# Kernel optimization log

Hardware: AMD Instinct MI355X
Metric: run time of the kernel (lower is better)

The kernel has to match this reference:

```python
import jax, jax.numpy as jnp
import numpy as np

R_MIN, R_MAX, MAX_PHASE = 0.9, 0.999, 6.283
BN_EPS = 1e-5


def _lru(x, nu_log, theta_log, B_re, B_im, C_re, C_im, D):
    # x: [B,T,E]; diagonal LRU with complex state of size H
    lam = jnp.exp(-jnp.exp(nu_log) + 1j * jnp.exp(theta_log))          # [H] complex
    gamma = jnp.sqrt(jnp.maximum(1.0 - jnp.abs(lam) ** 2, 1e-12))      # [H]
    Bc = B_re + 1j * B_im                                               # [H,E]
    Cc = C_re + 1j * C_im                                               # [E,H]
    Bu = jnp.einsum('bte,he->bth', x.astype(jnp.complex64), Bc) * gamma  # [B,T,H]

    def step(h, u):
        h = lam * h + u
        return h, h

    h0 = jnp.zeros((x.shape[0], lam.shape[0]), jnp.complex64)
    _, hs = jax.lax.scan(step, h0, jnp.swapaxes(Bu, 0, 1))              # [T,B,H]
    hs = jnp.swapaxes(hs, 0, 1)                                         # [B,T,H]
    return jnp.einsum('bth,eh->bte', hs, Cc).real + D * x               # [B,T,E]


def _batchnorm(x, scale, bias):
    # normalize over (batch, time), feature axis last
    mu = jnp.mean(x, axis=(0, 1))
    var = jnp.var(x, axis=(0, 1))
    return (x - mu) * jax.lax.rsqrt(var + BN_EPS) * scale + bias


def _glu(x):
    a, b = jnp.split(x, 2, axis=-1)
    return a * jax.nn.sigmoid(b)


def setup_inputs() -> dict:
    key = jax.random.key(0)
    ks = jax.random.split(key, 16)
    B, T, TS, E, H, L, O, NB = 32, 2048, 64, 256, 256, 1024, 10, 6
    u1 = jax.random.uniform(ks[0], (NB, H))
    u2 = jax.random.uniform(ks[1], (NB, H))
    nu_log = jnp.log(-0.5 * jnp.log(u1 * (R_MAX**2 - R_MIN**2) + R_MIN**2))
    theta_log = jnp.log(MAX_PHASE * u2)
    return {
        'x': jax.random.normal(ks[2], (B, T, TS), jnp.float32),
        'W_enc': jax.random.normal(ks[3], (TS, E), jnp.float32) / np.sqrt(TS),
        'b_enc': jnp.zeros((E,), jnp.float32),
        'nu_log': nu_log.astype(jnp.float32),
        'theta_log': theta_log.astype(jnp.float32),
        'B_re': jax.random.normal(ks[4], (NB, H, E), jnp.float32) / np.sqrt(2 * E),
        'B_im': jax.random.normal(ks[5], (NB, H, E), jnp.float32) / np.sqrt(2 * E),
        'C_re': jax.random.normal(ks[6], (NB, E, H), jnp.float32) / np.sqrt(H),
        'C_im': jax.random.normal(ks[7], (NB, E, H), jnp.float32) / np.sqrt(H),
        'D': jax.random.normal(ks[8], (NB, E), jnp.float32),
        'W1': jax.random.normal(ks[9], (NB, E, L), jnp.float32) / np.sqrt(E),
        'b1': jnp.zeros((NB, L), jnp.float32),
        'W2': jax.random.normal(ks[10], (NB, L // 2, E), jnp.float32) / np.sqrt(L // 2),
        'b2': jnp.zeros((NB, E), jnp.float32),
        'bn_scale': jnp.ones((NB, E), jnp.float32),
        'bn_bias': jnp.zeros((NB, E), jnp.float32),
        'W_out': jax.random.normal(ks[11], (E, O), jnp.float32) / np.sqrt(E),
        'b_out': jnp.zeros((O,), jnp.float32),
    }


def reference(x, W_enc, b_enc, nu_log, theta_log, B_re, B_im, C_re, C_im, D,
              W1, b1, W2, b2, bn_scale, bn_bias, W_out, b_out):
    x = x @ W_enc + b_enc                      # [B,T,E]
    y = x                                       # residual anchor (same for every block)
    for i in range(6):
        h = _batchnorm(x, bn_scale[i], bn_bias[i])
        h = _lru(h, nu_log[i], theta_log[i], B_re[i], B_im[i], C_re[i], C_im[i], D[i])
        h = _glu(h @ W1[i] + b1[i])             # dropout is identity (p=0 / eval)
        h = h @ W2[i] + b2[i]
        x = h + y
    pooled = jnp.mean(x, axis=1)                # pool=True head: mean over time
    return pooled @ W_out + b_out               # [B, out_dim]
```

## Files before the change

### kernel.cpp

```cpp
#include <hip/hip_runtime.h>
#include <hip/hip_bf16.h>
#include <math.h>

using bf16 = __hip_bfloat16;
typedef __attribute__((ext_vector_type(8))) short s8v;
typedef __attribute__((ext_vector_type(4))) float f4v;

#define MTOT 65536
#define TLEN 2048
#define NCHUNK 32
#define TCH 64

__device__ __forceinline__ float b2f(bf16 x) { return __bfloat162float(x); }
__device__ __forceinline__ bf16 f2b(float x) { return __float2bfloat16(x); }
__device__ __forceinline__ float bits2f(unsigned short u) {
    unsigned int x = ((unsigned int)u) << 16; float f; __builtin_memcpy(&f, &x, 4); return f;
}
__device__ __forceinline__ unsigned short f2bits(float x) {
    bf16 h = f2b(x); unsigned short u; __builtin_memcpy(&u, &h, 2); return u;
}

__device__ __forceinline__ float ldf(const void* p, size_t i, int f) {
    return f ? ((const float*)p)[i] : b2f(((const bf16*)p)[i]);
}

__device__ __forceinline__ void ld_g2l(const void* g, void* l) {
    __builtin_amdgcn_global_load_lds(
        (const __attribute__((address_space(1))) void*)g,
        (__attribute__((address_space(3))) void*)l,
        16, 0, 0);
}

__global__ void detect_k(const unsigned short* __restrict__ x, int* __restrict__ flag) {
    int tid = threadIdx.x;
    int cnt = 0;
    for (int i = tid; i < 8192; i += 256) {
        int e = (x[i] >> 7) & 0xFF;
        if (e == 0 || e == 0xFF) cnt++;
    }
    __shared__ int red[256];
    red[tid] = cnt;
    __syncthreads();
    for (int s = 128; s > 0; s >>= 1) {
        if (tid < s) red[tid] += red[tid + s];
        __syncthreads();
    }
    if (tid == 0) flag[0] = (red[0] >= 2) ? 1 : 0;
}

__global__ void cvt_k(const void* __restrict__ src, bf16* __restrict__ dst, int n,
                      const int* __restrict__ flag) {
    int f = *flag;
    int i = blockIdx.x * 256 + threadIdx.x;
    if (i < n) dst[i] = f2b(ldf(src, i, f));
}

__global__ void cvt_small(const void* b_enc, const void* Dp, const void* b1, const void* b2,
                          const void* bn_s, const void* bn_b, const void* W_out, const void* b_out,
                          bf16* b_encb, bf16* Db, bf16* b1b, bf16* b2b, bf16* bnsb, bf16* bnbb,
                          bf16* Woutb, bf16* boutb, const int* __restrict__ flag) {
    int f = *flag;
    int blk = blockIdx.x, t = threadIdx.x;
    const void* src; bf16* dst; int base, n;
    if (blk < 1)       { src = b_enc; dst = b_encb; base = blk;      n = 256; }
    else if (blk < 7)  { src = Dp;    dst = Db;     base = blk - 1;  n = 1536; }
    else if (blk < 31) { src = b1;    dst = b1b;    base = blk - 7;  n = 6144; }
    else if (blk < 37) { src = b2;    dst = b2b;    base = blk - 31; n = 1536; }
    else if (blk < 43) { src = bn_s;  dst = bnsb;   base = blk - 37; n = 1536; }
    else if (blk < 49) { src = bn_b;  dst = bnbb;   base = blk - 43; n = 1536; }
    else if (blk < 59) { src = W_out; dst = Woutb;  base = blk - 49; n = 2560; }
    else               { src = b_out; dst = boutb;  base = 0;        n = 10; }
    int i = base * 256 + t;
    if (i < n) dst[i] = f2b(ldf(src, i, f));
}

__global__ void lamgam_k(const void* __restrict__ nu, const void* __restrict__ th,
                         float* __restrict__ lamb, float* __restrict__ gamt,
                         const int* __restrict__ flag) {
    int f = *flag;
    int g = blockIdx.x * 256 + threadIdx.x;
    float nl = ldf(nu, g, f), tl = ldf(th, g, f);
    float mag = expf(-expf(nl));
    float ang = expf(tl);
    lamb[g * 2] = mag * cosf(ang);
    lamb[g * 2 + 1] = mag * sinf(ang);
    gamt[g] = sqrtf(fmaxf(1.f - mag * mag, 1e-12f));
}

template<int KK, int NBN, int EPI>
__global__ __launch_bounds__(256)
void gemm_v7(const bf16* __restrict__ A, const bf16* __restrict__ W,
             bf16* __restrict__ outB, bf16* __restrict__ outB2, int ldo,
             const bf16* __restrict__ bias,
             const bf16* __restrict__ Dv, const bf16* __restrict__ aux,
             const float* __restrict__ fstats, float* __restrict__ spart,
             const float* __restrict__ lamp, float* __restrict__ carry)
{
    constexpr int LG = (NBN == 8) ? 3 : 2;
    const int id = blockIdx.x;
    const int xcd = id & 7, q = id >> 3;
    const int bn = q & (NBN - 1);
    const int bm = (q >> LG) * 8 + xcd;

    const int tid = threadIdx.x;
    const int lane = tid & 63, wv = tid >> 6;
    const int wm = wv >> 1, wn = wv & 1;
    const int quad = lane >> 4, cl = lane & 15;

    __shared__ __align__(16) short As[3][128 * 32];
    __shared__ __align__(16) short Ws[3][64 * 32];
    __shared__ float sred[256];

    const char* Ab = (const char*)A + (size_t)bm * 128 * ((size_t)KK * 2);
    const char* Wb = (const char*)W + (size_t)bn * 64 * ((size_t)KK * 2);
    constexpr int ldb = KK * 2;

    auto stage = [&](int t, int bi) {
        const int kb = t * 64;
#pragma unroll
        for (int it = 0; it < 2; ++it) {
            int G = it * 256 + tid;
            int r = G >> 2;
            int gl = (G & 3) ^ ((r >> 1) & 3);
            ld_g2l(Ab + (size_t)r * ldb + kb + gl * 16,
                   (char*)As[bi] + (it * 4 + wv) * 1024);
        }
        {
            int r = tid >> 2;
            int gl = (tid & 3) ^ ((r >> 1) & 3);
            ld_g2l(Wb + (size_t)r * ldb + kb + gl * 16,
                   (char*)Ws[bi] + wv * 1024);
        }
    };

    f4v acc[4][2];
#pragma unroll
    for (int i = 0; i < 4; i++)
#pragma unroll
        for (int j = 0; j < 2; j++) acc[i][j] = (f4v){0.f, 0.f, 0.f, 0.f};

    constexpr int NT = KK >> 5;
    stage(0, 0);
    if (NT > 1) stage(1, 1);
#pragma unroll
    for (int t = 0; t < NT; ++t) {
        if (t + 2 < NT) {
            stage(t + 2, (t + 2) % 3);
            asm volatile("s_waitcnt vmcnt(6)" ::: "memory");
        } else if (t + 1 < NT) {
            asm volatile("s_waitcnt vmcnt(3)" ::: "memory");
        } else {
            asm volatile("s_waitcnt vmcnt(0)" ::: "memory");
        }
        asm volatile("s_barrier" ::: "memory");
        const char* Ac = (const char*)As[t % 3];
        const char* Wc = (const char*)Ws[t % 3];
        s8v af[4], bw[2];
#pragma unroll
        for (int i = 0; i < 4; i++) {
            int r = wm * 64 + i * 16 + cl;
            af[i] = *(const s8v*)(Ac + r * 64 + ((quad ^ ((r >> 1) & 3)) * 16));
        }
#pragma unroll
        for (int j = 0; j < 2; j++) {
            int r = wn * 32 + j * 16 + cl;
            bw[j] = *(const s8v*)(Wc + r * 64 + ((quad ^ ((r >> 1) & 3)) * 16));
        }
#pragma unroll
        for (int i = 0; i < 4; i++)
#pragma unroll
            for (int j = 0; j < 2; j++)
                acc[i][j] = __builtin_amdgcn_mfma_f32_16x16x32_bf16(af[i], bw[j], acc[i][j], 0, 0, 0);
        asm volatile("s_barrier" ::: "memory");
    }

    const size_t ld = (size_t)ldo;
    constexpr bool STATS = (EPI == 1 || EPI == 5);
#pragma unroll
    for (int j = 0; j < 2; j++) {
        float ss = 0.f, ss2 = 0.f;
        const int n = bn * 64 + wn * 32 + j * 16 + cl;
        float Er[4], Ei[4], Cr[4], Cim[4];
        if constexpr (EPI == 6) {
            int h = n >> 1;
            float lr = lamp[h * 2], li = lamp[h * 2 + 1];
            float a2r = lr * lr - li * li, a2i = 2.f * lr * li;
            float a3r = a2r * lr - a2i * li, a3i = a2r * li + a2i * lr;
            float l4r = a2r * a2r - a2i * a2i, l4i = 2.f * a2r * a2i;
            float l8r = l4r * l4r - l4i * l4i, l8i = 2.f * l4r * l4i;
            float l12r = l8r * l4r - l8i * l4i, l12i = l8r * l4i + l8i * l4r;
            float Br = (quad == 0) ? l12r : (quad == 1) ? l8r : (quad == 2) ? l4r : 1.f;
            float Bi = (quad == 0) ? l12i : (quad == 1) ? l8i : (quad == 2) ? l4i : 0.f;
            float Ar[4] = { a3r, a2r, lr, 1.f };
            float Ai[4] = { a3i, a2i, li, 0.f };
#pragma unroll
            for (int r4 = 0; r4 < 4; r4++) {
                Er[r4] = Ar[r4] * Br - Ai[r4] * Bi;
                Ei[r4] = Ar[r4] * Bi + Ai[r4] * Br;
            }
            float l16r = l12r * l4r - l12i * l4i, l16i = l12r * l4i + l12i * l4r;
            float l32r = l16r * l16r - l16i * l16i, l32i = 2.f * l16r * l16i;
            float l48r = l32r * l16r - l32i * l16i, l48i = l32r * l16i + l32i * l16r;
            Cr[0] = l48r; Cim[0] = l48i;
            Cr[1] = l32r; Cim[1] = l32i;
            Cr[2] = l16r; Cim[2] = l16i;
            Cr[3] = 1.f;  Cim[3] = 0.f;
        }
        float Sr = 0.f, Si = 0.f;
#pragma unroll
        for (int i = 0; i < 4; i++) {
#pragma unroll
            for (int r4 = 0; r4 < 4; r4++) {
                int m = bm * 128 + wm * 64 + i * 16 + quad * 4 + r4;
                size_t idx = (size_t)m * ld + n;
                float v = acc[i][j][r4];
                if (EPI == 1) {
                    v += b2f(bias[n]);
                    outB[idx] = f2b(v);
                    outB2[idx] = f2b(v);
                } else if (EPI == 2) {
                    v += b2f(Dv[n]) * (fstats[n] * b2f(aux[idx]) + fstats[256 + n]);
                    outB[idx] = f2b(v);
                } else if (EPI == 5) {
                    v += b2f(bias[n]) + b2f(aux[idx]);
                    outB[idx] = f2b(v);
                } else if (EPI == 6) {
                    v += fstats[n];
                    bf16 ob = f2b(v);
                    outB[idx] = ob;
                    float vr = b2f(ob);
                    float wr = Er[r4] * Cr[i] - Ei[r4] * Cim[i];
                    float wi = Er[r4] * Cim[i] + Ei[r4] * Cr[i];
                    Sr += vr * wr;
                    Si += vr * wi;
                }
                if (STATS) { ss += v; ss2 += v * v; }
            }
        }
        if constexpr (EPI == 6) {
            Sr += __shfl_xor(Sr, 16); Sr += __shfl_xor(Sr, 32);
            Si += __shfl_xor(Si, 16); Si += __shfl_xor(Si, 32);
            float pSr = __shfl_xor(Sr, 1), pSi = __shfl_xor(Si, 1);
            if (quad == 0 && (cl & 1) == 0) {
                size_t gc = (size_t)(bm * 2 + wm);
                size_t ci = (gc * 256 + (size_t)(n >> 1)) * 2;
                carry[ci]     = Sr - pSi;
                carry[ci + 1] = Si + pSr;
            }
        }
        if (STATS) {
            ss += __shfl_xor(ss, 16);  ss += __shfl_xor(ss, 32);
            ss2 += __shfl_xor(ss2, 16); ss2 += __shfl_xor(ss2, 32);
            if (lane < 16) {
                int nl = wn * 32 + j * 16 + lane;
                sred[wm * 64 + nl] = ss;
                sred[128 + wm * 64 + nl] = ss2;
            }
        }
    }
    if constexpr (STATS) {
        __syncthreads();
        if (tid < 64) {
            float sv = sred[tid] + sred[64 + tid];
            float sv2 = sred[128 + tid] + sred[192 + tid];
            spart[(size_t)bm * 256 + bn * 64 + tid] = sv;
            spart[131072 + (size_t)bm * 256 + bn * 64 + tid] = sv2;
        }
    }
}

__global__ __launch_bounds__(256)
void glu_v7(const bf16* __restrict__ A, const bf16* __restrict__ W,
            bf16* __restrict__ outB, const bf16* __restrict__ bias)
{
    constexpr int KK = 256;
    const int id = blockIdx.x;
    const int xcd = id & 7, q = id >> 3;
    const int nb = q & 7;
    const int bm = (q >> 3) * 8 + xcd;

    const int tid = threadIdx.x;
    const int lane = tid & 63, wv = tid >> 6;
    const int wm = wv >> 1, wn = wv & 1;
    const int quad = lane >> 4, cl = lane & 15;

    __shared__ __align__(16) short As[3][128 * 32];
    __shared__ __align__(16) short Vs[3][64 * 32];
    __shared__ __align__(16) short Gs[3][64 * 32];

    const char* Ab = (const char*)A + (size_t)bm * 128 * ((size_t)KK * 2);
    const char* Vb = (const char*)W + (size_t)(nb * 64) * ((size_t)KK * 2);
    const char* Gb = (const char*)W + (size_t)(512 + nb * 64) * ((size_t)KK * 2);
    constexpr int ldb = KK * 2;

    auto stage = [&](int t, int bi) {
        const int kb = t * 64;
#pragma unroll
        for (int it = 0; it < 2; ++it) {
            int G = it * 256 + tid;
            int r = G >> 2;
            int gl = (G & 3) ^ ((r >> 1) & 3);
            ld_g2l(Ab + (size_t)r * ldb + kb + gl * 16,
                   (char*)As[bi] + (it * 4 + wv) * 1024);
        }
        {
            int r = tid >> 2;
            int gl = (tid & 3) ^ ((r >> 1) & 3);
            ld_g2l(Vb + (size_t)r * ldb + kb + gl * 16, (char*)Vs[bi] + wv * 1024);
            ld_g2l(Gb + (size_t)r * ldb + kb + gl * 16, (char*)Gs[bi] + wv * 1024);
        }
    };

    f4v accv[4][2], accg[4][2];
#pragma unroll
    for (int i = 0; i < 4; i++)
#pragma unroll
        for (int j = 0; j < 2; j++) {
            accv[i][j] = (f4v){0.f, 0.f, 0.f, 0.f};
            accg[i][j] = (f4v){0.f, 0.f, 0.f, 0.f};
        }

    constexpr int NT = KK >> 5;
    stage(0, 0);
    stage(1, 1);
#pragma unroll
    for (int t = 0; t < NT; ++t) {
        if (t + 2 < NT) {
            stage(t + 2, (t + 2) % 3);
            asm volatile("s_waitcnt vmcnt(8)" ::: "memory");
        } else if (t + 1 < NT) {
            asm volatile("s_waitcnt vmcnt(4)" ::: "memory");
        } else {
            asm volatile("s_waitcnt vmcnt(0)" ::: "memory");
        }
        asm volatile("s_barrier" ::: "memory");
        const char* Ac = (const char*)As[t % 3];
        const char* Vc = (const char*)Vs[t % 3];
        const char* Gc = (const char*)Gs[t % 3];
        s8v af[4], bv[2], bg[2];
#pragma unroll
        for (int i = 0; i < 4; i++) {
            int r = wm * 64 + i * 16 + cl;
            af[i] = *(const s8v*)(Ac + r * 64 + ((quad ^ ((r >> 1) & 3)) * 16));
        }
#pragma unroll
        for (int j = 0; j < 2; j++) {
            int r = wn * 32 + j * 16 + cl;
            int off = r * 64 + ((quad ^ ((r >> 1) & 3)) * 16);
            bv[j] = *(const s8v*)(Vc + off);
            bg[j] = *(const s8v*)(Gc + off);
        }
#pragma unroll
        for (int i = 0; i < 4; i++)
#pragma unroll
            for (int j = 0; j < 2; j++) {
                accv[i][j] = __builtin_amdgcn_mfma_f32_16x16x32_bf16(af[i], bv[j], accv[i][j], 0, 0, 0);
                accg[i][j] = __builtin_amdgcn_mfma_f32_16x16x32_bf16(af[i], bg[j], accg[i][j], 0, 0, 0);
            }
        asm volatile("s_barrier" ::: "memory");
    }

#pragma unroll
    for (int i = 0; i < 4; i++) {
#pragma unroll
        for (int j = 0; j < 2; j++) {
#pragma unroll
            for (int r4 = 0; r4 < 4; r4++) {
                int m = bm * 128 + wm * 64 + i * 16 + quad * 4 + r4;
                int n = nb * 64 + wn * 32 + j * 16 + cl;
                float v = accv[i][j][r4] + b2f(bias[n]);
                float g = accg[i][j][r4] + b2f(bias[512 + n]);
                outB[(size_t)m * 512 + n] = f2b(v * (1.f / (1.f + __expf(-g))));
            }
        }
    }
}

__global__ void bn_finish2(const float* __restrict__ part, float* __restrict__ stats,
                           const bf16* __restrict__ sc, const bf16* __restrict__ bi) {
    int e = blockIdx.x;
    int t = threadIdx.x;
    float s = part[(size_t)t * 256 + e] + part[(size_t)(t + 256) * 256 + e];
    float s2 = part[131072 + (size_t)t * 256 + e] + part[131072 + (size_t)(t + 256) * 256 + e];
    __shared__ float rs[256], rs2[256];
    rs[t] = s; rs2[t] = s2;
    __syncthreads();
    for (int k = 128; k > 0; k >>= 1) {
        if (t < k) { rs[t] += rs[t + k]; rs2[t] += rs2[t + k]; }
        __syncthreads();
    }
    if (t == 0) {
        float mu = rs[0] * (1.f / 65536.f);
        float var = rs2[0] * (1.f / 65536.f) - mu * mu;
        float a = rsqrtf(var + 1e-5f) * b2f(sc[e]);
        stats[e] = a;
        stats[256 + e] = b2f(bi[e]) - mu * a;
    }
}

__global__ void pack_wb(const void* __restrict__ B_re, const void* __restrict__ B_im,
                        size_t off, const float* __restrict__ gam,
                        const float* __restrict__ stats,
                        bf16* __restrict__ out, float* __restrict__ bias_out,
                        const int* __restrict__ flag) {
    int f = *flag;
    int n = blockIdx.x;
    int e = threadIdx.x;
    int h = n >> 1;
    const void* src = (n & 1) ? B_im : B_re;
    float v = ldf(src, off + (size_t)h * 256 + e, f);
    out[(size_t)n * 256 + e] = f2b(v * gam[h] * stats[e]);
    __shared__ float rs[256];
    rs[e] = v * stats[256 + e];
    __syncthreads();
    for (int k = 128; k > 0; k >>= 1) {
        if (e < k) rs[e] += rs[e + k];
        __syncthreads();
    }
    if (e == 0) bias_out[n] = rs[0] * gam[h];
}

__global__ void pack_all(const void* __restrict__ C_re, const void* __restrict__ C_im,
                         const void* __restrict__ W1, const void* __restrict__ W2,
                         bf16* __restrict__ wc6, bf16* __restrict__ w1t6, bf16* __restrict__ w2t6,
                         const int* __restrict__ flag) {
    int f = *flag;
    int L = blockIdx.x >> 11;
    int blk = blockIdx.x & 2047;
    size_t offC = (size_t)L * 65536, offW1 = (size_t)L * 262144, offW2 = (size_t)L * 131072;
    if (blk < 512) {
        int g = blk * 256 + threadIdx.x;
        int e = g >> 9, k = g & 511, h = k >> 1;
        float v = ldf((k & 1) ? C_im : C_re, offC + (size_t)e * 256 + h, f);
        wc6[(size_t)L * 131072 + g] = f2b((k & 1) ? -v : v);
    } else if (blk < 1536) {
        int g = (blk - 512) * 256 + threadIdx.x;
        int n = g >> 8, k = g & 255;
        w1t6[(size_t)L * 262144 + g] = f2b(ldf(W1, offW1 + (size_t)k * 1024 + n, f));
    } else {
        int g = (blk - 1536) * 256 + threadIdx.x;
        int n = g >> 9, k = g & 511;
        w2t6[(size_t)L * 131072 + g] = f2b(ldf(W2, offW2 + (size_t)k * 256 + n, f));
    }
}

__global__ void lru_prefix(const float* __restrict__ carry, float* __restrict__ pre,
                           const float* __restrict__ lam) {
    int g = blockIdx.x * 256 + threadIdx.x;
    int h = g & 255, b = g >> 8;
    float pr = lam[h * 2], pi = lam[h * 2 + 1];
    for (int k = 0; k < 6; k++) { float nr = pr * pr - pi * pi; pi = 2.f * pr * pi; pr = nr; }
    float er = 0.f, ei = 0.f;
    for (int c = 0; c < NCHUNK; c++) {
        size_t idx = ((size_t)(b * NCHUNK + c) * 256 + h) * 2;
        pre[idx] = er; pre[idx + 1] = ei;
        float cr = carry[idx], ci = carry[idx + 1];
        float nr = pr * er - pi * ei + cr;
        ei = pr * ei + pi * er + ci;
        er = nr;
    }
}

__global__ void lru_final(bf16* __restrict__ bu, const float* __restrict__ pre,
                          const float* __restrict__ lam) {
    int gg = blockIdx.x * 256 + threadIdx.x;
    int hp = gg & 127, c = (gg >> 7) & 31, b = gg >> 12;
    f4v lm = *(const f4v*)&lam[hp * 4];
    f4v st = *(const f4v*)&pre[(size_t)gg * 4];
    float sr0 = st[0], si0 = st[1], sr1 = st[2], si1 = st[3];
    char* p = (char*)(bu + ((size_t)(b * TLEN + c * TCH)) * 512) + hp * 8;
    for (int t = 0; t < TCH; t++) {
        unsigned long long u = *(const unsigned long long*)p;
        float ur0 = bits2f((unsigned short)u), ui0 = bits2f((unsigned short)(u >> 16));
        float ur1 = bits2f((unsigned short)(u >> 32)), ui1 = bits2f((unsigned short)(u >> 48));
        float nr0 = lm[0] * sr0 - lm[1] * si0 + ur0;
        si0 = lm[0] * si0 + lm[1] * sr0 + ui0; sr0 = nr0;
        float nr1 = lm[2] * sr1 - lm[3] * si1 + ur1;
        si1 = lm[2] * si1 + lm[3] * sr1 + ui1; sr1 = nr1;
        unsigned long long w = (unsigned long long)f2bits(sr0)
                             | ((unsigned long long)f2bits(si0) << 16)
                             | ((unsigned long long)f2bits(sr1) << 32)
                             | ((unsigned long long)f2bits(si1) << 48);
        *(unsigned long long*)p = w;
        p += 1024;
    }
}

__global__ void head_k(const float* __restrict__ part, const bf16* __restrict__ W_out,
                       const bf16* __restrict__ b_out, void* __restrict__ out,
                       const int* __restrict__ flag) {
    int b = blockIdx.x;
    int tid = threadIdx.x;
    __shared__ float sp[256];
    __shared__ float red[160];
    float s = 0.f;
    for (int c = 0; c < 16; c++) s += part[((size_t)(b * 16 + c)) * 256 + tid];
    sp[tid] = s * (1.f / 2048.f);
    __syncthreads();
    if (tid < 160) {
        int o = tid >> 4, sg = tid & 15;
        float a = 0.f;
        for (int e = sg; e < 256; e += 16) a += sp[e] * b2f(W_out[e * 10 + o]);
        red[tid] = a;
    }
    __syncthreads();
    if (tid < 10) {
        float acc = b2f(b_out[tid]);
        for (int sg = 0; sg < 16; sg++) acc += red[tid * 16 + sg];
        if (*flag) ((float*)out)[b * 10 + tid] = acc;
        else       ((bf16*)out)[b * 10 + tid] = f2b(acc);
    }
}

__global__ void pack_wt_enc(const void* __restrict__ W_enc, bf16* __restrict__ out,
                            const int* __restrict__ flag) {
    int f = *flag;
    int g = blockIdx.x * 256 + threadIdx.x;
    int n = g >> 6, k = g & 63;
    out[g] = f2b(ldf(W_enc, (size_t)k * 256 + n, f));
}

extern "C" void kernel_launch(void* const* d_in, const int* in_sizes, int n_in,
                              void* d_out, int out_size, void* d_ws, size_t ws_size,
                              hipStream_t stream) {
    (void)in_sizes; (void)n_in; (void)out_size; (void)ws_size;
    const void* x      = d_in[0];
    const void* W_enc  = d_in[1];
    const void* b_enc  = d_in[2];
    const void* nu_log = d_in[3];
    const void* th_log = d_in[4];
    const void* B_re   = d_in[5];
    const void* B_im   = d_in[6];
    const void* C_re   = d_in[7];
    const void* C_im   = d_in[8];
    const void* Dp     = d_in[9];
    const void* W1     = d_in[10];
    const void* b1     = d_in[11];
    const void* W2     = d_in[12];
    const void* b2     = d_in[13];
    const void* bn_s   = d_in[14];
    const void* bn_b   = d_in[15];
    const void* W_out  = d_in[16];
    const void* b_out  = d_in[17];

    char* w = (char*)d_ws;
    bf16* xc  = (bf16*)w; w += (size_t)MTOT * 256 * 2;
    bf16* y   = (bf16*)w; w += (size_t)MTOT * 256 * 2;
    bf16* hbn = (bf16*)w; w += (size_t)MTOT * 256 * 2;
    bf16* bu  = (bf16*)w; w += (size_t)MTOT * 512 * 2;
    float* stats  = (float*)w; w += 4096;
    float* bnpart = (float*)w; w += 1048576;
    float* carry  = (float*)w; w += 2097152;
    float* pre    = (float*)w; w += 2097152;
    float* lamb   = (float*)w; w += 12288;
    float* gamt   = (float*)w; w += 6144;
    float* bubias = (float*)w; w += 2048;
    int*   flag   = (int*)w;  w += 256;
    bf16* wt_enc = (bf16*)w; w += 32768;
    bf16* wb   = (bf16*)w; w += 262144;
    bf16* wc6  = (bf16*)w; w += 6 * 262144;
    bf16* w1t6 = (bf16*)w; w += 6 * 524288;
    bf16* w2t6 = (bf16*)w; w += 6 * 262144;
    bf16* b_encb = (bf16*)w; w += 512;
    bf16* Db     = (bf16*)w; w += 3072;
    bf16* b1b    = (bf16*)w; w += 12288;
    bf16* b2b    = (bf16*)w; w += 3072;
    bf16* bnsb   = (bf16*)w; w += 3072;
    bf16* bnbb   = (bf16*)w; w += 3072;
    bf16* Woutb  = (bf16*)w; w += 5120;
    bf16* boutb  = (bf16*)w; w += 32;
    bf16* xb = bu;

    dim3 blk(256);
    detect_k<<<1, blk, 0, stream>>>((const unsigned short*)x, flag);
    cvt_k<<<16384, blk, 0, stream>>>(x, xb, 4194304, flag);
    cvt_small<<<60, blk, 0, stream>>>(b_enc, Dp, b1, b2, bn_s, bn_b, W_out, b_out,
                                      b_encb, Db, b1b, b2b, bnsb, bnbb, Woutb, boutb, flag);
    lamgam_k<<<6, blk, 0, stream>>>(nu_log, th_log, lamb, gamt, flag);
    pack_wt_enc<<<64, blk, 0, stream>>>(W_enc, wt_enc, flag);
    pack_all<<<12288, blk, 0, stream>>>(C_re, C_im, W1, W2, wc6, w1t6, w2t6, flag);

    gemm_v7<64, 4, 1><<<2048, blk, 0, stream>>>(xb, wt_enc, xc, y, 256,
                                                b_encb, nullptr, nullptr, nullptr, bnpart,
                                                nullptr, nullptr);
    for (int i = 0; i < 6; ++i) {
        bn_finish2<<<256, blk, 0, stream>>>(bnpart, stats, bnsb + i * 256, bnbb + i * 256);
        pack_wb<<<512, blk, 0, stream>>>(B_re, B_im, (size_t)i * 65536, gamt + i * 256,
                                         stats, wb, bubias, flag);
        gemm_v7<256, 8, 6><<<4096, blk, 0, stream>>>(xc, wb, bu, nullptr, 512,
                                                     nullptr, nullptr, nullptr, bubias, nullptr,
                                                     lamb + i * 512, carry);
        lru_prefix<<<32, blk, 0, stream>>>(carry, pre, lamb + i * 512);
        lru_final<<<512, blk, 0, stream>>>(bu, pre, lamb + i * 512);
        gemm_v7<512, 4, 2><<<2048, blk, 0, stream>>>(bu, wc6 + (size_t)i * 131072, hbn, nullptr, 256,
                                                     nullptr, Db + i * 256, xc, stats, nullptr,
                                                     nullptr, nullptr);
        glu_v7<<<4096, blk, 0, stream>>>(hbn, w1t6 + (size_t)i * 262144, bu, b1b + i * 1024);
        gemm_v7<512, 4, 5><<<2048, blk, 0, stream>>>(bu, w2t6 + (size_t)i * 131072, xc, nullptr, 256,
                                                     b2b + i * 256, nullptr, y, nullptr, bnpart,
                                                     nullptr, nullptr);
    }
    head_k<<<32, blk, 0, stream>>>(bnpart, Woutb, boutb, d_out, flag);
}
```

Before: 1.390 ms.

## Process two M-tiles per GLU block, fold LRU prefix into final, vectorize cvt

```diff
diff --git a/kernel.cpp b/kernel.cpp
--- a/kernel.cpp
+++ b/kernel.cpp
@@ -48,11 +48,16 @@
     if (tid == 0) flag[0] = (red[0] >= 2) ? 1 : 0;
 }
 
-__global__ void cvt_k(const void* __restrict__ src, bf16* __restrict__ dst, int n,
-                      const int* __restrict__ flag) {
+__global__ void cvt_k4(const void* __restrict__ src, bf16* __restrict__ dst, int n,
+                       const int* __restrict__ flag) {
     int f = *flag;
-    int i = blockIdx.x * 256 + threadIdx.x;
-    if (i < n) dst[i] = f2b(ldf(src, i, f));
+    int i = (blockIdx.x * 256 + threadIdx.x) * 4;
+    if (i + 3 < n) {
+#pragma unroll
+        for (int k = 0; k < 4; k++) dst[i + k] = f2b(ldf(src, i + k, f));
+    } else {
+        for (int k = 0; k < 4 && i + k < n; k++) dst[i + k] = f2b(ldf(src, i + k, f));
+    }
 }
 
 __global__ void cvt_small(const void* b_enc, const void* Dp, const void* b1, const void* b2,
@@ -270,14 +275,15 @@
 }
 
 __global__ __launch_bounds__(256)
-void glu_v7(const bf16* __restrict__ A, const bf16* __restrict__ W,
+void glu_v8(const bf16* __restrict__ A, const bf16* __restrict__ W,
             bf16* __restrict__ outB, const bf16* __restrict__ bias)
 {
     constexpr int KK = 256;
+    constexpr int GT = 16;
     const int id = blockIdx.x;
     const int xcd = id & 7, q = id >> 3;
     const int nb = q & 7;
-    const int bm = (q >> 3) * 8 + xcd;
+    const int mgrp = (q >> 3) * 8 + xcd;
 
     const int tid = threadIdx.x;
     const int lane = tid & 63, wv = tid >> 6;
@@ -288,18 +294,21 @@
     __shared__ __align__(16) short Vs[3][64 * 32];
     __shared__ __align__(16) short Gs[3][64 * 32];
 
-    const char* Ab = (const char*)A + (size_t)bm * 128 * ((size_t)KK * 2);
+    const char* Abase = (const char*)A;
     const char* Vb = (const char*)W + (size_t)(nb * 64) * ((size_t)KK * 2);
     const char* Gb = (const char*)W + (size_t)(512 + nb * 64) * ((size_t)KK * 2);
     constexpr int ldb = KK * 2;
 
-    auto stage = [&](int t, int bi) {
-        const int kb = t * 64;
+    auto stage = [&](int G) {
+        const int tile = G >> 3;
+        const int kb = (G & 7) * 64;
+        const int bi = G % 3;
+        const char* Ab = Abase + (size_t)(mgrp * 2 + tile) * 128 * ((size_t)KK * 2);
 #pragma unroll
         for (int it = 0; it < 2; ++it) {
-            int G = it * 256 + tid;
-            int r = G >> 2;
-            int gl = (G & 3) ^ ((r >> 1) & 3);
+            int Gt = it * 256 + tid;
+            int r = Gt >> 2;
+            int gl = (Gt & 3) ^ ((r >> 1) & 3);
             ld_g2l(Ab + (size_t)r * ldb + kb + gl * 16,
                    (char*)As[bi] + (it * 4 + wv) * 1024);
         }
@@ -320,23 +329,22 @@
             accg[i][j] = (f4v){0.f, 0.f, 0.f, 0.f};
         }
 
-    constexpr int NT = KK >> 5;
-    stage(0, 0);
-    stage(1, 1);
-#pragma unroll
-    for (int t = 0; t < NT; ++t) {
-        if (t + 2 < NT) {
-            stage(t + 2, (t + 2) % 3);
+    stage(0);
+    stage(1);
+#pragma unroll
+    for (int G = 0; G < GT; ++G) {
+        if (G + 2 < GT) {
+            stage(G + 2);
             asm volatile("s_waitcnt vmcnt(8)" ::: "memory");
-        } else if (t + 1 < NT) {
+        } else if (G + 1 < GT) {
             asm volatile("s_waitcnt vmcnt(4)" ::: "memory");
         } else {
             asm volatile("s_waitcnt vmcnt(0)" ::: "memory");
         }
         asm volatile("s_barrier" ::: "memory");
-        const char* Ac = (const char*)As[t % 3];
-        const char* Vc = (const char*)Vs[t % 3];
-        const char* Gc = (const char*)Gs[t % 3];
+        const char* Ac = (const char*)As[G % 3];
+        const char* Vc = (const char*)Vs[G % 3];
+        const char* Gc = (const char*)Gs[G % 3];
         s8v af[4], bv[2], bg[2];
 #pragma unroll
         for (int i = 0; i < 4; i++) {
@@ -358,19 +366,31 @@
                 accg[i][j] = __builtin_amdgcn_mfma_f32_16x16x32_bf16(af[i], bg[j], accg[i][j], 0, 0, 0);
             }
         asm volatile("s_barrier" ::: "memory");
-    }
-
-#pragma unroll
-    for (int i = 0; i < 4; i++) {
-#pragma unroll
-        for (int j = 0; j < 2; j++) {
-#pragma unroll
-            for (int r4 = 0; r4 < 4; r4++) {
-                int m = bm * 128 + wm * 64 + i * 16 + quad * 4 + r4;
-                int n = nb * 64 + wn * 32 + j * 16 + cl;
-                float v = accv[i][j][r4] + b2f(bias[n]);
-                float g = accg[i][j][r4] + b2f(bias[512 + n]);
-                outB[(size_t)m * 512 + n] = f2b(v * (1.f / (1.f + __expf(-g))));
+
+        if ((G & 7) == 7) {
+            const int bm = mgrp * 2 + (G >> 3);
+#pragma unroll
+            for (int i = 0; i < 4; i++) {
+#pragma unroll
+                for (int j = 0; j < 2; j++) {
+#pragma unroll
+                    for (int r4 = 0; r4 < 4; r4++) {
+                        int m = bm * 128 + wm * 64 + i * 16 + quad * 4 + r4;
+                        int n = nb * 64 + wn * 32 + j * 16 + cl;
+                        float v = accv[i][j][r4] + b2f(bias[n]);
+                        float g = accg[i][j][r4] + b2f(bias[512 + n]);
+                        outB[(size_t)m * 512 + n] = f2b(v * (1.f / (1.f + __expf(-g))));
+                    }
+                }
+            }
+            if (G + 1 < GT) {
+#pragma unroll
+                for (int i = 0; i < 4; i++)
+#pragma unroll
+                    for (int j = 0; j < 2; j++) {
+                        accv[i][j] = (f4v){0.f, 0.f, 0.f, 0.f};
+                        accg[i][j] = (f4v){0.f, 0.f, 0.f, 0.f};
+                    }
             }
         }
     }
@@ -444,30 +464,27 @@
     }
 }
 
-__global__ void lru_prefix(const float* __restrict__ carry, float* __restrict__ pre,
-                           const float* __restrict__ lam) {
-    int g = blockIdx.x * 256 + threadIdx.x;
-    int h = g & 255, b = g >> 8;
-    float pr = lam[h * 2], pi = lam[h * 2 + 1];
-    for (int k = 0; k < 6; k++) { float nr = pr * pr - pi * pi; pi = 2.f * pr * pi; pr = nr; }
-    float er = 0.f, ei = 0.f;
-    for (int c = 0; c < NCHUNK; c++) {
-        size_t idx = ((size_t)(b * NCHUNK + c) * 256 + h) * 2;
-        pre[idx] = er; pre[idx + 1] = ei;
-        float cr = carry[idx], ci = carry[idx + 1];
-        float nr = pr * er - pi * ei + cr;
-        ei = pr * ei + pi * er + ci;
-        er = nr;
-    }
-}
-
-__global__ void lru_final(bf16* __restrict__ bu, const float* __restrict__ pre,
+__global__ void lru_final(bf16* __restrict__ bu, const float* __restrict__ carry,
                           const float* __restrict__ lam) {
     int gg = blockIdx.x * 256 + threadIdx.x;
     int hp = gg & 127, c = (gg >> 7) & 31, b = gg >> 12;
     f4v lm = *(const f4v*)&lam[hp * 4];
-    f4v st = *(const f4v*)&pre[(size_t)gg * 4];
-    float sr0 = st[0], si0 = st[1], sr1 = st[2], si1 = st[3];
+    float q0r = lm[0], q0i = lm[1], q1r = lm[2], q1i = lm[3];
+#pragma unroll
+    for (int k = 0; k < 6; k++) {
+        float n0 = q0r * q0r - q0i * q0i; q0i = 2.f * q0r * q0i; q0r = n0;
+        float n1 = q1r * q1r - q1i * q1i; q1i = 2.f * q1r * q1i; q1r = n1;
+    }
+    float sr0 = 0.f, si0 = 0.f, sr1 = 0.f, si1 = 0.f;
+    const f4v* cp = (const f4v*)(carry + ((size_t)b * 32) * 512) + hp;
+    for (int cc = 0; cc < c; cc++) {
+        f4v cv = *cp;
+        float n0 = q0r * sr0 - q0i * si0 + cv[0];
+        si0 = q0r * si0 + q0i * sr0 + cv[1]; sr0 = n0;
+        float n1 = q1r * sr1 - q1i * si1 + cv[2];
+        si1 = q1r * si1 + q1i * sr1 + cv[3]; sr1 = n1;
+        cp += 128;
+    }
     char* p = (char*)(bu + ((size_t)(b * TLEN + c * TCH)) * 512) + hp * 8;
     for (int t = 0; t < TCH; t++) {
         unsigned long long u = *(const unsigned long long*)p;
@@ -551,7 +568,6 @@
     float* stats  = (float*)w; w += 4096;
     float* bnpart = (float*)w; w += 1048576;
     float* carry  = (float*)w; w += 2097152;
-    float* pre    = (float*)w; w += 2097152;
     float* lamb   = (float*)w; w += 12288;
     float* gamt   = (float*)w; w += 6144;
     float* bubias = (float*)w; w += 2048;
@@ -573,7 +589,7 @@
 
     dim3 blk(256);
     detect_k<<<1, blk, 0, stream>>>((const unsigned short*)x, flag);
-    cvt_k<<<16384, blk, 0, stream>>>(x, xb, 4194304, flag);
+    cvt_k4<<<4096, blk, 0, stream>>>(x, xb, 4194304, flag);
     cvt_small<<<60, blk, 0, stream>>>(b_enc, Dp, b1, b2, bn_s, bn_b, W_out, b_out,
                                       b_encb, Db, b1b, b2b, bnsb, bnbb, Woutb, boutb, flag);
     lamgam_k<<<6, blk, 0, stream>>>(nu_log, th_log, lamb, gamt, flag);
@@ -590,12 +606,11 @@
         gemm_v7<256, 8, 6><<<4096, blk, 0, stream>>>(xc, wb, bu, nullptr, 512,
                                                      nullptr, nullptr, nullptr, bubias, nullptr,
                                                      lamb + i * 512, carry);
-        lru_prefix<<<32, blk, 0, stream>>>(carry, pre, lamb + i * 512);
-        lru_final<<<512, blk, 0, stream>>>(bu, pre, lamb + i * 512);
+        lru_final<<<512, blk, 0, stream>>>(bu, carry, lamb + i * 512);
         gemm_v7<512, 4, 2><<<2048, blk, 0, stream>>>(bu, wc6 + (size_t)i * 131072, hbn, nullptr, 256,
                                                      nullptr, Db + i * 256, xc, stats, nullptr,
                                                      nullptr, nullptr);
-        glu_v7<<<4096, blk, 0, stream>>>(hbn, w1t6 + (size_t)i * 262144, bu, b1b + i * 1024);
+        glu_v8<<<2048, blk, 0, stream>>>(hbn, w1t6 + (size_t)i * 262144, bu, b1b + i * 1024);
         gemm_v7<512, 4, 5><<<2048, blk, 0, stream>>>(bu, w2t6 + (size_t)i * 131072, xc, nullptr, 256,
                                                      b2b + i * 256, nullptr, y, nullptr, bnpart,
                                                      nullptr, nullptr);
```

Result: no change. 1.384 ms (-0.4%).
